# Kernel tuning notes

Measured on AMD Instinct MI355X. Metric: run time of the kernel, lower is better.

Reference implementation:

```python
import jax, jax.numpy as jnp
import numpy as np

DIM = 4096
N_HEADS = 32
N_KV_HEADS = 8
HEAD_DIM = 128
WINDOW = 4096
BATCH = 32
START_POS = 4095


def setup_inputs() -> dict:
    key = jax.random.key(0)
    ks = jax.random.split(key, 8)
    x = jax.random.normal(ks[0], (BATCH, DIM), dtype=jnp.float32)
    wqkv = jax.random.normal(ks[1], (DIM, (N_HEADS + 2 * N_KV_HEADS) * HEAD_DIM), dtype=jnp.float32) * 0.02
    wo = jax.random.normal(ks[2], (N_HEADS * HEAD_DIM, DIM), dtype=jnp.float32) * 0.02
    cos = jax.random.uniform(ks[3], (HEAD_DIM,), dtype=jnp.float32)
    sin = jax.random.uniform(ks[4], (HEAD_DIM,), dtype=jnp.float32)
    cache_k = jax.random.normal(ks[5], (BATCH, N_KV_HEADS, WINDOW, HEAD_DIM), dtype=jnp.float32)
    cache_v = jax.random.normal(ks[6], (BATCH, N_KV_HEADS, WINDOW, HEAD_DIM), dtype=jnp.float32)
    mask = jnp.zeros((BATCH, 1, 1, WINDOW), dtype=jnp.float32)
    return {"x": x, "wqkv": wqkv, "wo": wo, "cos": cos, "sin": sin,
            "cache_k": cache_k, "cache_v": cache_v, "mask": mask,
            "start_pos": START_POS}


def _rotate_half(t):
    t1, t2 = jnp.split(t, 2, axis=-1)
    return jnp.concatenate([-t2, t1], axis=-1)


def _rope(t, cos, sin):
    # t: [..., head_dim]; cos/sin: [head_dim] at the current decode position
    return t * cos + _rotate_half(t) * sin


def reference(x, wqkv, wo, cos, sin, cache_k, cache_v, mask, start_pos):
    B, D = x.shape
    KV = cache_k.shape[1]
    Hd = cache_k.shape[3]
    window = cache_k.shape[2]
    H = wo.shape[0] // Hd
    R = H // KV  # GQA repeats
    scale = 1.0 / np.sqrt(Hd)

    # fused QKV projection (matmul_1d + nlp_create_qkv_heads)
    qkv = x @ wqkv  # [B, (H+2*KV)*Hd]
    q = qkv[:, : H * Hd].reshape(B, H, Hd)
    k = qkv[:, H * Hd : (H + KV) * Hd].reshape(B, KV, Hd)
    v = qkv[:, (H + KV) * Hd :].reshape(B, KV, Hd)

    # rotary embedding on q and k at current position
    q = _rope(q, cos, sin)
    k = _rope(k, cos, sin)

    # sliding-window KV cache update at current_pos
    cur = start_pos % window  # python int
    cache_k = cache_k.at[:, :, cur].set(k)
    cache_v = cache_v.at[:, :, cur].set(v)

    # unpad to padded_layer_past_len = min(nearest_32(start_pos+1), window)
    padded_len = min(((start_pos + 1 + 31) // 32) * 32, window)
    keys = cache_k[:, :, :padded_len]   # [B, KV, T, Hd]
    values = cache_v[:, :, :padded_len]

    # grouped-query attention: q -> [B, KV, R, Hd]
    qg = q.reshape(B, KV, R, Hd)
    scores = jnp.einsum("bgrd,bgtd->bgrt", qg, keys) * scale  # [B, KV, R, T]
    scores = scores + mask[:, :, :, :padded_len]  # broadcast over kv-heads/repeats
    attn = jax.nn.softmax(scores, axis=-1)
    out = jnp.einsum("bgrt,bgtd->bgrd", attn, values)  # [B, KV, R, Hd]

    # concat heads + output projection
    out = out.reshape(B, H * Hd)
    return out @ wo  # [B, D]
```

## Files before the change

### kernel.cpp

```cpp
#include <hip/hip_runtime.h>
#include <math.h>

#define DIM 4096
#define NH 32
#define NKV 8
#define HD 128
#define WINDOW 4096
#define BATCH 32
#define QKV_N 6144
#define ATTN_SCALE 0.08838834764831845f
#define CHUNK 256
#define NC 16
#define SLICES 16

__device__ __forceinline__ float4 f4max(float4 a, float4 b) {
  return make_float4(fmaxf(a.x, b.x), fmaxf(a.y, b.y), fmaxf(a.z, b.z), fmaxf(a.w, b.w));
}
__device__ __forceinline__ float4 f4add(float4 a, float4 b) {
  return make_float4(a.x + b.x, a.y + b.y, a.z + b.z, a.w + b.w);
}
__device__ __forceinline__ void fma4(float4& a, float4 x, float4 y) {
  a.x = fmaf(x.x, y.x, a.x); a.y = fmaf(x.y, y.y, a.y);
  a.z = fmaf(x.z, y.z, a.z); a.w = fmaf(x.w, y.w, a.w);
}
__device__ __forceinline__ void fma4s(float4& a, float s, float4 v) {
  a.x = fmaf(s, v.x, a.x); a.y = fmaf(s, v.y, a.y);
  a.z = fmaf(s, v.z, a.z); a.w = fmaf(s, v.w, a.w);
}
__device__ __forceinline__ float4 wred_max(float4 v) {
#pragma unroll
  for (int o = 1; o < 64; o <<= 1) {
    v.x = fmaxf(v.x, __shfl_xor(v.x, o));
    v.y = fmaxf(v.y, __shfl_xor(v.y, o));
    v.z = fmaxf(v.z, __shfl_xor(v.z, o));
    v.w = fmaxf(v.w, __shfl_xor(v.w, o));
  }
  return v;
}
__device__ __forceinline__ float4 wred_add(float4 v) {
#pragma unroll
  for (int o = 1; o < 64; o <<= 1) {
    v.x += __shfl_xor(v.x, o);
    v.y += __shfl_xor(v.y, o);
    v.z += __shfl_xor(v.z, o);
    v.w += __shfl_xor(v.w, o);
  }
  return v;
}

template<int N, int K, int NS>
__global__ __launch_bounds__(256)
void gemm_part(const float* __restrict__ x, const float* __restrict__ w,
               float* __restrict__ part) {
  const int t = threadIdx.x;
  const int c0 = blockIdx.x * 64 + (t & 15) * 4;
  const int r0 = (t >> 4) * 2;
  const int kn = K / NS;
  const int ks = blockIdx.y * kn;

  float a00 = 0.f, a01 = 0.f, a02 = 0.f, a03 = 0.f;
  float a10 = 0.f, a11 = 0.f, a12 = 0.f, a13 = 0.f;

  const float* xr0 = x + (size_t)r0 * K;
  const float* xr1 = xr0 + K;
  const float* wp = w + (size_t)ks * N + c0;

  for (int k = ks; k < ks + kn; k += 4) {
    float4 xa = *(const float4*)(xr0 + k);
    float4 xb = *(const float4*)(xr1 + k);
    float xav[4] = {xa.x, xa.y, xa.z, xa.w};
    float xbv[4] = {xb.x, xb.y, xb.z, xb.w};
#pragma unroll
    for (int kk = 0; kk < 4; ++kk) {
      float4 wv = *(const float4*)(wp);
      wp += N;
      a00 = fmaf(xav[kk], wv.x, a00);
      a01 = fmaf(xav[kk], wv.y, a01);
      a02 = fmaf(xav[kk], wv.z, a02);
      a03 = fmaf(xav[kk], wv.w, a03);
      a10 = fmaf(xbv[kk], wv.x, a10);
      a11 = fmaf(xbv[kk], wv.y, a11);
      a12 = fmaf(xbv[kk], wv.z, a12);
      a13 = fmaf(xbv[kk], wv.w, a13);
    }
  }
  float* p = part + ((size_t)blockIdx.y * 32 + r0) * N + c0;
  *(float4*)p = make_float4(a00, a01, a02, a03);
  *(float4*)(p + N) = make_float4(a10, a11, a12, a13);
}

__global__ __launch_bounds__(256)
void rope_reduce(const float* __restrict__ part, const float* __restrict__ cosv,
                 const float* __restrict__ sinv, float* __restrict__ q,
                 float* __restrict__ knew, float* __restrict__ vnew) {
  int idx = blockIdx.x * 256 + threadIdx.x;
  int r = idx / 3072;
  int rem = idx - r * 3072;
  int head = rem >> 6;
  int d = rem & 63;
  int c1 = head * 128 + d;
  int c2 = c1 + 64;
  float v1 = 0.f, v2 = 0.f;
#pragma unroll
  for (int s = 0; s < SLICES; ++s) {
    v1 += part[((size_t)s * 32 + r) * QKV_N + c1];
    v2 += part[((size_t)s * 32 + r) * QKV_N + c2];
  }
  if (head < NH + NKV) {
    float c_lo = cosv[d], c_hi = cosv[d + 64];
    float s_lo = sinv[d], s_hi = sinv[d + 64];
    float o1 = v1 * c_lo - v2 * s_lo;
    float o2 = v2 * c_hi + v1 * s_hi;
    if (head < NH) {
      q[((size_t)r * NH + head) * HD + d] = o1;
      q[((size_t)r * NH + head) * HD + d + 64] = o2;
    } else {
      int g = head - NH;
      knew[((size_t)r * NKV + g) * HD + d] = o1;
      knew[((size_t)r * NKV + g) * HD + d + 64] = o2;
    }
  } else {
    int g = head - NH - NKV;
    vnew[((size_t)r * NKV + g) * HD + d] = v1;
    vnew[((size_t)r * NKV + g) * HD + d + 64] = v2;
  }
}

__global__ __launch_bounds__(256)
void attn_chunk(const float* __restrict__ q, const float* __restrict__ knew,
                const float* __restrict__ vnew, const float* __restrict__ cache_k,
                const float* __restrict__ cache_v, const float* __restrict__ mask,
                const int* __restrict__ start_pos_p,
                float* __restrict__ pvp, float* __restrict__ msp) {
  const int bg = blockIdx.x;
  const int b = bg >> 3;
  const int c = blockIdx.y;
  const int t = threadIdx.x;
  const int w = t >> 6;
  const int sp = start_pos_p[0];
  const int cur = sp & (WINDOW - 1);
  int plen = ((sp + 1 + 31) >> 5) << 5;
  if (plen > WINDOW) plen = WINDOW;
  const int t0 = c * CHUNK;
  const int tend = min(t0 + CHUNK, plen);

  const size_t msbase = (((size_t)c * 256 + bg) * 4) * 2;
  float* pvb = pvp + (((size_t)c * 256 + bg) * 4) * HD;

  __shared__ __align__(16) float q_s[4][HD];
  __shared__ __align__(16) float s_lds[CHUNK][4];
  __shared__ __align__(16) float4 red_s[8];
  __shared__ __align__(16) float scratch[8 * 512];

  if (t0 >= plen) {
    if (t < 8) msp[msbase + t] = (t & 1) ? 0.f : -1e30f;
    for (int i = t; i < 4 * HD; i += 256) pvb[i] = 0.f;
    return;
  }

  for (int i = t; i < 512; i += 256) {
    int h = i >> 7, d = i & 127;
    q_s[h][d] = q[((size_t)b * NH + ((bg & 7) * 4 + h)) * HD + d];
  }
  __syncthreads();

  const float* kbase = cache_k + (size_t)bg * WINDOW * HD;
  const float* vbase = cache_v + (size_t)bg * WINDOW * HD;
  const float* krow_new = knew + (size_t)bg * HD;
  const float* vrow_new = vnew + (size_t)bg * HD;

  {
    const int p0 = t >> 2;
    const int dl = t & 3;
    for (int tt = t0 + p0; tt < t0 + CHUNK; tt += 64) {
      if (tt < tend) {
        const float* krow = (tt == cur) ? krow_new : (kbase + (size_t)tt * HD);
        float4 a0 = {0,0,0,0}, a1 = {0,0,0,0}, a2 = {0,0,0,0}, a3 = {0,0,0,0};
#pragma unroll
        for (int j = 0; j < 8; ++j) {
          const int f = dl + 4 * j;
          float4 kv = *(const float4*)(krow + 4 * f);
          fma4(a0, kv, *(const float4*)(&q_s[0][4 * f]));
          fma4(a1, kv, *(const float4*)(&q_s[1][4 * f]));
          fma4(a2, kv, *(const float4*)(&q_s[2][4 * f]));
          fma4(a3, kv, *(const float4*)(&q_s[3][4 * f]));
        }
        float s0 = a0.x + a0.y + a0.z + a0.w;
        float s1 = a1.x + a1.y + a1.z + a1.w;
        float s2 = a2.x + a2.y + a2.z + a2.w;
        float s3 = a3.x + a3.y + a3.z + a3.w;
        s0 += __shfl_xor(s0, 1); s0 += __shfl_xor(s0, 2);
        s1 += __shfl_xor(s1, 1); s1 += __shfl_xor(s1, 2);
        s2 += __shfl_xor(s2, 1); s2 += __shfl_xor(s2, 2);
        s3 += __shfl_xor(s3, 1); s3 += __shfl_xor(s3, 2);
        float sv = (dl == 0) ? s0 : (dl == 1) ? s1 : (dl == 2) ? s2 : s3;
        s_lds[tt - t0][dl] = sv * ATTN_SCALE + mask[(size_t)b * WINDOW + tt];
      } else {
        s_lds[tt - t0][dl] = -1e30f;
      }
    }
  }
  __syncthreads();

  float4 sval = *(const float4*)(s_lds[t]);
  float4 m = wred_max(sval);
  if ((t & 63) == 0) red_s[w] = m;
  __syncthreads();
  float4 mx = f4max(f4max(red_s[0], red_s[1]), f4max(red_s[2], red_s[3]));

  float4 e;
  e.x = __expf(sval.x - mx.x);
  e.y = __expf(sval.y - mx.y);
  e.z = __expf(sval.z - mx.z);
  e.w = __expf(sval.w - mx.w);
  *(float4*)(s_lds[t]) = e;
  float4 s = wred_add(e);
  if ((t & 63) == 0) red_s[4 + w] = s;
  __syncthreads();
  if (t == 0) {
    float4 sm = f4add(f4add(red_s[4], red_s[5]), f4add(red_s[6], red_s[7]));
    msp[msbase + 0] = mx.x; msp[msbase + 1] = sm.x;
    msp[msbase + 2] = mx.y; msp[msbase + 3] = sm.y;
    msp[msbase + 4] = mx.z; msp[msbase + 5] = sm.z;
    msp[msbase + 6] = mx.w; msp[msbase + 7] = sm.w;
  }

  {
    const int d4 = t & 31;
    const int toff = t >> 5;
    float4 a0 = {0,0,0,0}, a1 = {0,0,0,0}, a2 = {0,0,0,0}, a3 = {0,0,0,0};
    for (int tt = t0 + toff; tt < tend; tt += 8) {
      const float* vrow = (tt == cur) ? vrow_new : (vbase + (size_t)tt * HD);
      float4 vv = *(const float4*)(vrow + 4 * d4);
      float4 p = *(const float4*)(s_lds[tt - t0]);
      fma4s(a0, p.x, vv);
      fma4s(a1, p.y, vv);
      fma4s(a2, p.z, vv);
      fma4s(a3, p.w, vv);
    }
    *(float4*)(&scratch[(toff * 4 + 0) * HD + 4 * d4]) = a0;
    *(float4*)(&scratch[(toff * 4 + 1) * HD + 4 * d4]) = a1;
    *(float4*)(&scratch[(toff * 4 + 2) * HD + 4 * d4]) = a2;
    *(float4*)(&scratch[(toff * 4 + 3) * HD + 4 * d4]) = a3;
  }
  __syncthreads();
  for (int i = t; i < 4 * HD; i += 256) {
    float s2 = 0.f;
#pragma unroll
    for (int o = 0; o < 8; ++o) s2 += scratch[o * 512 + i];
    pvb[i] = s2;
  }
}

__global__ __launch_bounds__(256)
void attn_combine(const float* __restrict__ pvp, const float* __restrict__ msp,
                  float* __restrict__ attn_out) {
  int idx = blockIdx.x * 256 + threadIdx.x;
  int b = idx >> 12;
  int rem = idx & 4095;
  int hf = rem >> 7;
  int d = rem & 127;
  int g = hf >> 2, hh = hf & 3;
  int bg = b * 8 + g;
  float mv[NC], sv[NC];
  float M = -1e30f;
#pragma unroll
  for (int c = 0; c < NC; ++c) {
    mv[c] = msp[(((size_t)c * 256 + bg) * 4 + hh) * 2];
    sv[c] = msp[(((size_t)c * 256 + bg) * 4 + hh) * 2 + 1];
    M = fmaxf(M, mv[c]);
  }
  float num = 0.f, den = 0.f;
#pragma unroll
  for (int c = 0; c < NC; ++c) {
    float w = __expf(mv[c] - M);
    den = fmaf(sv[c], w, den);
    num = fmaf(pvp[(((size_t)c * 256 + bg) * 4 + hh) * HD + d], w, num);
  }
  attn_out[idx] = num / den;
}

__global__ __launch_bounds__(256)
void reduce_out(const float* __restrict__ part, float* __restrict__ out) {
  int idx = blockIdx.x * 256 + threadIdx.x;
  float s = 0.f;
#pragma unroll
  for (int sl = 0; sl < SLICES; ++sl) s += part[(size_t)sl * 32 * DIM + idx];
  out[idx] = s;
}

extern "C" void kernel_launch(void* const* d_in, const int* in_sizes, int n_in,
                              void* d_out, int out_size, void* d_ws, size_t ws_size,
                              hipStream_t stream) {
  const float* x       = (const float*)d_in[0];
  const float* wqkv    = (const float*)d_in[1];
  const float* wo      = (const float*)d_in[2];
  const float* cosv    = (const float*)d_in[3];
  const float* sinv    = (const float*)d_in[4];
  const float* cache_k = (const float*)d_in[5];
  const float* cache_v = (const float*)d_in[6];
  const float* mask    = (const float*)d_in[7];
  const int*   start_p = (const int*)d_in[8];
  float* ws = (float*)d_ws;

  float* part     = ws;
  float* q        = ws + 3145728;
  float* knew     = q + 131072;
  float* vnew     = knew + 32768;
  float* attn_out = vnew + 32768;
  float* pvp      = attn_out + 131072;
  float* msp      = pvp + 2097152;
  float* out      = (float*)d_out;

  gemm_part<QKV_N, DIM, SLICES><<<dim3(QKV_N / 64, SLICES), 256, 0, stream>>>(x, wqkv, part);
  rope_reduce<<<384, 256, 0, stream>>>(part, cosv, sinv, q, knew, vnew);
  attn_chunk<<<dim3(BATCH * NKV, NC), 256, 0, stream>>>(q, knew, vnew, cache_k,
                                                        cache_v, mask, start_p,
                                                        pvp, msp);
  attn_combine<<<512, 256, 0, stream>>>(pvp, msp, attn_out);
  gemm_part<DIM, DIM, SLICES><<<dim3(DIM / 64, SLICES), 256, 0, stream>>>(attn_out, wo, part);
  reduce_out<<<512, 256, 0, stream>>>(part, out);
}
```

Measured before the change: 364.2 us.

## Give each wavefront its own attention chunk to remove block-level syncs

The attention kernel now gives each 64-lane wavefront an independent 128-token chunk, doubling the number of split-K chunks to 32. This removes all __syncthreads and the shared-memory scratch reduction in favour of in-wave shuffles. The combine kernel switches to an online-softmax merge over the larger number of partials. The trade-off is more partial output written to and read from global memory, plus a larger workspace footprint.

```diff
diff --git a/kernel.cpp b/kernel.cpp
--- a/kernel.cpp
+++ b/kernel.cpp
@@ -9,8 +9,8 @@
 #define BATCH 32
 #define QKV_N 6144
 #define ATTN_SCALE 0.08838834764831845f
-#define CHUNK 256
-#define NC 16
+#define WCHUNK 128
+#define NCW 32
 #define SLICES 16
 
 __device__ __forceinline__ float4 f4max(float4 a, float4 b) {
@@ -46,6 +46,12 @@
     v.w += __shfl_xor(v.w, o);
   }
   return v;
+}
+__device__ __forceinline__ void xor32_add(float4& v) {
+  v.x += __shfl_xor(v.x, 32);
+  v.y += __shfl_xor(v.y, 32);
+  v.z += __shfl_xor(v.z, 32);
+  v.w += __shfl_xor(v.w, 32);
 }
 
 template<int N, int K, int NS>
@@ -126,43 +132,44 @@
   }
 }
 
-__global__ __launch_bounds__(256)
-void attn_chunk(const float* __restrict__ q, const float* __restrict__ knew,
-                const float* __restrict__ vnew, const float* __restrict__ cache_k,
-                const float* __restrict__ cache_v, const float* __restrict__ mask,
-                const int* __restrict__ start_pos_p,
-                float* __restrict__ pvp, float* __restrict__ msp) {
+__global__ __launch_bounds__(256, 5)
+void attn_wave(const float* __restrict__ q, const float* __restrict__ knew,
+               const float* __restrict__ vnew, const float* __restrict__ cache_k,
+               const float* __restrict__ cache_v, const float* __restrict__ mask,
+               const int* __restrict__ start_pos_p,
+               float* __restrict__ pvp, float* __restrict__ msp) {
   const int bg = blockIdx.x;
   const int b = bg >> 3;
-  const int c = blockIdx.y;
-  const int t = threadIdx.x;
-  const int w = t >> 6;
+  const int w = threadIdx.x >> 6;
+  const int lane = threadIdx.x & 63;
+  const int c = blockIdx.y * 4 + w;
   const int sp = start_pos_p[0];
   const int cur = sp & (WINDOW - 1);
   int plen = ((sp + 1 + 31) >> 5) << 5;
   if (plen > WINDOW) plen = WINDOW;
-  const int t0 = c * CHUNK;
-  const int tend = min(t0 + CHUNK, plen);
-
-  const size_t msbase = (((size_t)c * 256 + bg) * 4) * 2;
-  float* pvb = pvp + (((size_t)c * 256 + bg) * 4) * HD;
-
-  __shared__ __align__(16) float q_s[4][HD];
-  __shared__ __align__(16) float s_lds[CHUNK][4];
-  __shared__ __align__(16) float4 red_s[8];
-  __shared__ __align__(16) float scratch[8 * 512];
+  const int t0 = c * WCHUNK;
+  const int tend = min(t0 + WCHUNK, plen);
+
+  const size_t pidx = ((size_t)c * 256 + bg) * 4;
+  float* pvb = pvp + pidx * HD;
+  float* msb = msp + pidx * 2;
+
+  __shared__ __align__(16) float q_s[4][4 * HD];
+  __shared__ __align__(16) float s_s[4][WCHUNK][4];
 
   if (t0 >= plen) {
-    if (t < 8) msp[msbase + t] = (t & 1) ? 0.f : -1e30f;
-    for (int i = t; i < 4 * HD; i += 256) pvb[i] = 0.f;
+    if (lane < 8) msb[lane] = (lane & 1) ? 0.f : -1e30f;
+    for (int i = lane; i < 4 * HD; i += 64) pvb[i] = 0.f;
     return;
   }
 
-  for (int i = t; i < 512; i += 256) {
-    int h = i >> 7, d = i & 127;
-    q_s[h][d] = q[((size_t)b * NH + ((bg & 7) * 4 + h)) * HD + d];
-  }
-  __syncthreads();
+  {
+    const float* qsrc = q + ((size_t)b * NH + (bg & 7) * 4) * HD;
+    float4 v0 = *(const float4*)(qsrc + lane * 8);
+    float4 v1 = *(const float4*)(qsrc + lane * 8 + 4);
+    *(float4*)(&q_s[w][lane * 8]) = v0;
+    *(float4*)(&q_s[w][lane * 8 + 4]) = v1;
+  }
 
   const float* kbase = cache_k + (size_t)bg * WINDOW * HD;
   const float* vbase = cache_v + (size_t)bg * WINDOW * HD;
@@ -170,9 +177,9 @@
   const float* vrow_new = vnew + (size_t)bg * HD;
 
   {
-    const int p0 = t >> 2;
-    const int dl = t & 3;
-    for (int tt = t0 + p0; tt < t0 + CHUNK; tt += 64) {
+    const int p0 = lane >> 2;
+    const int dl = lane & 3;
+    for (int tt = t0 + p0; tt < t0 + WCHUNK; tt += 16) {
       if (tt < tend) {
         const float* krow = (tt == cur) ? krow_new : (kbase + (size_t)tt * HD);
         float4 a0 = {0,0,0,0}, a1 = {0,0,0,0}, a2 = {0,0,0,0}, a3 = {0,0,0,0};
@@ -180,10 +187,10 @@
         for (int j = 0; j < 8; ++j) {
           const int f = dl + 4 * j;
           float4 kv = *(const float4*)(krow + 4 * f);
-          fma4(a0, kv, *(const float4*)(&q_s[0][4 * f]));
-          fma4(a1, kv, *(const float4*)(&q_s[1][4 * f]));
-          fma4(a2, kv, *(const float4*)(&q_s[2][4 * f]));
-          fma4(a3, kv, *(const float4*)(&q_s[3][4 * f]));
+          fma4(a0, kv, *(const float4*)(&q_s[w][0 * HD + 4 * f]));
+          fma4(a1, kv, *(const float4*)(&q_s[w][1 * HD + 4 * f]));
+          fma4(a2, kv, *(const float4*)(&q_s[w][2 * HD + 4 * f]));
+          fma4(a3, kv, *(const float4*)(&q_s[w][3 * HD + 4 * f]));
         }
         float s0 = a0.x + a0.y + a0.z + a0.w;
         float s1 = a1.x + a1.y + a1.z + a1.w;
@@ -194,61 +201,51 @@
         s2 += __shfl_xor(s2, 1); s2 += __shfl_xor(s2, 2);
         s3 += __shfl_xor(s3, 1); s3 += __shfl_xor(s3, 2);
         float sv = (dl == 0) ? s0 : (dl == 1) ? s1 : (dl == 2) ? s2 : s3;
-        s_lds[tt - t0][dl] = sv * ATTN_SCALE + mask[(size_t)b * WINDOW + tt];
+        s_s[w][tt - t0][dl] = sv * ATTN_SCALE + mask[(size_t)b * WINDOW + tt];
       } else {
-        s_lds[tt - t0][dl] = -1e30f;
+        s_s[w][tt - t0][dl] = -1e30f;
       }
     }
   }
-  __syncthreads();
-
-  float4 sval = *(const float4*)(s_lds[t]);
-  float4 m = wred_max(sval);
-  if ((t & 63) == 0) red_s[w] = m;
-  __syncthreads();
-  float4 mx = f4max(f4max(red_s[0], red_s[1]), f4max(red_s[2], red_s[3]));
-
-  float4 e;
-  e.x = __expf(sval.x - mx.x);
-  e.y = __expf(sval.y - mx.y);
-  e.z = __expf(sval.z - mx.z);
-  e.w = __expf(sval.w - mx.w);
-  *(float4*)(s_lds[t]) = e;
-  float4 s = wred_add(e);
-  if ((t & 63) == 0) red_s[4 + w] = s;
-  __syncthreads();
-  if (t == 0) {
-    float4 sm = f4add(f4add(red_s[4], red_s[5]), f4add(red_s[6], red_s[7]));
-    msp[msbase + 0] = mx.x; msp[msbase + 1] = sm.x;
-    msp[msbase + 2] = mx.y; msp[msbase + 3] = sm.y;
-    msp[msbase + 4] = mx.z; msp[msbase + 5] = sm.z;
-    msp[msbase + 6] = mx.w; msp[msbase + 7] = sm.w;
+
+  float4 r0 = *(const float4*)(s_s[w][lane]);
+  float4 r1 = *(const float4*)(s_s[w][lane + 64]);
+  float4 mx = wred_max(f4max(r0, r1));
+  float4 e0, e1;
+  e0.x = __expf(r0.x - mx.x); e0.y = __expf(r0.y - mx.y);
+  e0.z = __expf(r0.z - mx.z); e0.w = __expf(r0.w - mx.w);
+  e1.x = __expf(r1.x - mx.x); e1.y = __expf(r1.y - mx.y);
+  e1.z = __expf(r1.z - mx.z); e1.w = __expf(r1.w - mx.w);
+  *(float4*)(s_s[w][lane]) = e0;
+  *(float4*)(s_s[w][lane + 64]) = e1;
+  float4 sm = wred_add(f4add(e0, e1));
+  if (lane == 0) {
+    msb[0] = mx.x; msb[1] = sm.x;
+    msb[2] = mx.y; msb[3] = sm.y;
+    msb[4] = mx.z; msb[5] = sm.z;
+    msb[6] = mx.w; msb[7] = sm.w;
   }
 
   {
-    const int d4 = t & 31;
-    const int toff = t >> 5;
+    const int d4 = lane & 31;
+    const int half = lane >> 5;
     float4 a0 = {0,0,0,0}, a1 = {0,0,0,0}, a2 = {0,0,0,0}, a3 = {0,0,0,0};
-    for (int tt = t0 + toff; tt < tend; tt += 8) {
+    for (int tt = t0 + half; tt < tend; tt += 2) {
       const float* vrow = (tt == cur) ? vrow_new : (vbase + (size_t)tt * HD);
       float4 vv = *(const float4*)(vrow + 4 * d4);
-      float4 p = *(const float4*)(s_lds[tt - t0]);
+      float4 p = *(const float4*)(s_s[w][tt - t0]);
       fma4s(a0, p.x, vv);
       fma4s(a1, p.y, vv);
       fma4s(a2, p.z, vv);
       fma4s(a3, p.w, vv);
     }
-    *(float4*)(&scratch[(toff * 4 + 0) * HD + 4 * d4]) = a0;
-    *(float4*)(&scratch[(toff * 4 + 1) * HD + 4 * d4]) = a1;
-    *(float4*)(&scratch[(toff * 4 + 2) * HD + 4 * d4]) = a2;
-    *(float4*)(&scratch[(toff * 4 + 3) * HD + 4 * d4]) = a3;
-  }
-  __syncthreads();
-  for (int i = t; i < 4 * HD; i += 256) {
-    float s2 = 0.f;
-#pragma unroll
-    for (int o = 0; o < 8; ++o) s2 += scratch[o * 512 + i];
-    pvb[i] = s2;
+    xor32_add(a0); xor32_add(a1); xor32_add(a2); xor32_add(a3);
+    if (half == 0) {
+      *(float4*)(&pvb[0 * HD + 4 * d4]) = a0;
+      *(float4*)(&pvb[1 * HD + 4 * d4]) = a1;
+      *(float4*)(&pvb[2 * HD + 4 * d4]) = a2;
+      *(float4*)(&pvb[3 * HD + 4 * d4]) = a3;
+    }
   }
 }
 
@@ -262,20 +259,19 @@
   int d = rem & 127;
   int g = hf >> 2, hh = hf & 3;
   int bg = b * 8 + g;
-  float mv[NC], sv[NC];
-  float M = -1e30f;
-#pragma unroll
-  for (int c = 0; c < NC; ++c) {
-    mv[c] = msp[(((size_t)c * 256 + bg) * 4 + hh) * 2];
-    sv[c] = msp[(((size_t)c * 256 + bg) * 4 + hh) * 2 + 1];
-    M = fmaxf(M, mv[c]);
-  }
-  float num = 0.f, den = 0.f;
-#pragma unroll
-  for (int c = 0; c < NC; ++c) {
-    float w = __expf(mv[c] - M);
-    den = fmaf(sv[c], w, den);
-    num = fmaf(pvp[(((size_t)c * 256 + bg) * 4 + hh) * HD + d], w, num);
+  float M = -1e30f, den = 0.f, num = 0.f;
+#pragma unroll 4
+  for (int c = 0; c < NCW; ++c) {
+    size_t base = ((size_t)c * 256 + bg) * 4 + hh;
+    float m = msp[base * 2];
+    float s = msp[base * 2 + 1];
+    float p = pvp[base * HD + d];
+    float Mn = fmaxf(M, m);
+    float so = __expf(M - Mn);
+    float sn = __expf(m - Mn);
+    den = den * so + s * sn;
+    num = num * so + p * sn;
+    M = Mn;
   }
   attn_out[idx] = num / den;
 }
@@ -309,14 +305,14 @@
   float* vnew     = knew + 32768;
   float* attn_out = vnew + 32768;
   float* pvp      = attn_out + 131072;
-  float* msp      = pvp + 2097152;
+  float* msp      = pvp + 4194304;
   float* out      = (float*)d_out;
 
   gemm_part<QKV_N, DIM, SLICES><<<dim3(QKV_N / 64, SLICES), 256, 0, stream>>>(x, wqkv, part);
   rope_reduce<<<384, 256, 0, stream>>>(part, cosv, sinv, q, knew, vnew);
-  attn_chunk<<<dim3(BATCH * NKV, NC), 256, 0, stream>>>(q, knew, vnew, cache_k,
-                                                        cache_v, mask, start_p,
-                                                        pvp, msp);
+  attn_wave<<<dim3(BATCH * NKV, NCW / 4), 256, 0, stream>>>(q, knew, vnew, cache_k,
+                                                            cache_v, mask, start_p,
+                                                            pvp, msp);
   attn_combine<<<512, 256, 0, stream>>>(pvp, msp, attn_out);
   gemm_part<DIM, DIM, SLICES><<<dim3(DIM / 64, SLICES), 256, 0, stream>>>(attn_out, wo, part);
   reduce_out<<<512, 256, 0, stream>>>(part, out);
```

Result: no change. 368.6 us (+1.2%).
